# Optimization experiments

Hardware: AMD Instinct MI355X
Metric: run time of the kernel (lower is better)

## Reference

```python
import jax, jax.numpy as jnp
import numpy as np
import math

B, C, N, L = 32, 128, 2048, 1
H, DK, APT = 8, 16, 10
EPS = 1e-5


def conv1x1(x, W, b):
    # 1x1 Conv2d on [B, C, N, L]
    return jnp.einsum('oc,bcnl->bonl', W, x) + b[None, :, None, None]


def layer_norm_12(x):
    # normalize over dims (1, 2) as in the custom LayerNorm (no affine)
    mean = x.mean(axis=(1, 2), keepdims=True)
    var = x.var(axis=(1, 2), keepdims=True)
    return (x - mean) / jnp.sqrt(var + EPS)


def setup_inputs() -> dict:
    key = jax.random.key(0)
    ks = jax.random.split(key, 10)
    s = 0.05  # small-scale init for numerical stability
    inp = {
        'input': jax.random.normal(ks[0], (B, C, N, L), jnp.float32),
        'Wq': jax.random.normal(ks[1], (C, C), jnp.float32) * s,
        'bq': jnp.zeros((C,), jnp.float32),
        'Wv': jax.random.normal(ks[2], (C, C), jnp.float32) * s,
        'bv': jnp.zeros((C,), jnp.float32),
        'Wc': jax.random.normal(ks[3], (C, C), jnp.float32) * s,
        'bc': jnp.zeros((C,), jnp.float32),
        'memory': jax.random.normal(ks[4], (H, L, N, DK), jnp.float32) * s,
        'sa_weight': jnp.ones((C, N, L), jnp.float32),
        'sa_bias': jnp.zeros((C, N, L), jnp.float32),
        'nodevec1': jax.random.normal(ks[5], (N, APT), jnp.float32),
        'nodevec2': jax.random.normal(ks[6], (APT, N), jnp.float32),
        'Wg1': jax.random.normal(ks[7], (C, C), jnp.float32) * s,
        'bg1': jnp.zeros((C,), jnp.float32),
        'Wg2': jax.random.normal(ks[8], (C, C), jnp.float32) * s,
        'bg2': jnp.zeros((C,), jnp.float32),
        'Wg3': jax.random.normal(ks[9], (C, C), jnp.float32) * s,
        'bg3': jnp.zeros((C,), jnp.float32),
    }
    return inp


def reference(input, Wq, bq, Wv, bv, Wc, bc, memory, sa_weight, sa_bias,
              nodevec1, nodevec2, Wg1, bg1, Wg2, bg2, Wg3, bg3):
    scale = math.sqrt(DK)

    def split_heads(t):  # [B,C,N,L] -> [B,H,L,N,DK]
        return t.reshape(B, H, DK, N, L).transpose(0, 1, 4, 3, 2)

    # SpatialAttention (Conv = 1x1 conv + relu; dropout off in eval)
    q = jax.nn.relu(conv1x1(input, Wq, bq))
    v = jax.nn.relu(conv1x1(input, Wv, bv))
    query = jax.nn.softmax(split_heads(q) / scale, axis=-1)     # [B,H,L,N,DK]
    value = split_heads(v)                                       # [B,H,L,N,DK]
    key = jax.nn.softmax(memory / scale, axis=-1)                # [H,L,N,DK]
    Aapt = jax.nn.softmax(jax.nn.relu(nodevec1 @ nodevec2), axis=-1)  # [N,N]

    kv = jnp.einsum('hlnx,bhlny->bhlxy', key, value)             # [B,H,L,DK,DK]
    attn_qkv = jnp.einsum('bhlnx,bhlxy->bhlny', query, kv)       # [B,H,L,N,DK]
    attn_dyn = jnp.einsum('nm,bhlnc->bhlnc', Aapt, value)        # row-sum scaling
    x = attn_qkv + attn_dyn

    # merge heads back to [B,C,N,L] and apply concat conv (Conv = conv+relu)
    x = x.transpose(0, 1, 4, 3, 2).reshape(B, C, N, L)
    x = jax.nn.relu(conv1x1(x, Wc, bc))
    x = x * sa_weight[None] + sa_bias[None] + x                  # affine branch

    # Encoder wrap
    x = x + input
    x = layer_norm_12(x)
    g = conv1x1(x, Wg1, bg1) * jax.nn.sigmoid(conv1x1(x, Wg2, bg2))
    g = conv1x1(g, Wg3, bg3)                                     # GLU
    x = g + x
    x = x * sa_weight[None] + sa_bias[None] + x
    x = layer_norm_12(x)
    return x
```

## Files before the change

kernel.cpp:

```cpp
#include <hip/hip_runtime.h>
#include <hip/hip_bf16.h>
#include <math.h>

#define DI __device__ __forceinline__

typedef short bf16x8 __attribute__((ext_vector_type(8)));
typedef float f32x4 __attribute__((ext_vector_type(4)));

constexpr int BB = 32, CC = 128, NN = 2048;
constexpr float EPSf = 1e-5f;
constexpr float RCN = 1.0f / (CC * (float)NN);

#define MFMA(a,b,c) __builtin_amdgcn_mfma_f32_16x16x32_bf16(a,b,c,0,0,0)

DI unsigned short f2b(float f){
    union { __hip_bfloat16 h; unsigned short u; } v;
    v.h = __float2bfloat16(f);
    return v.u;
}
DI float b2f(unsigned short h){
    union { unsigned u; float f; } v; v.u = ((unsigned)h) << 16;
    return v.f;
}
DI float sigm(float x){ return 1.0f / (1.0f + __expf(-x)); }

__global__ __launch_bounds__(256) void k_prep(
    const float* __restrict__ Wq, const float* __restrict__ Wv,
    const float* __restrict__ Wc, const float* __restrict__ Wg1,
    const float* __restrict__ Wg2, const float* __restrict__ Wg3,
    const float* __restrict__ mem,
    unsigned short* __restrict__ Wb, float* __restrict__ rs,
    unsigned short* __restrict__ ksT)
{
    const int tid = threadIdx.x;
    if (blockIdx.x < 96) {
        const int i = blockIdx.x * 256 + tid;
        const int m = i >> 12, q = i & 4095;
        const float* src = (m==0)?Wq:(m==1)?Wv:(m==2)?Wc:(m==3)?Wg1:(m==4)?Wg2:Wg3;
        f32x4 w = *(const f32x4*)&src[q * 4];
        ushort4 p; p.x=f2b(w[0]); p.y=f2b(w[1]); p.z=f2b(w[2]); p.w=f2b(w[3]);
        *(ushort4*)&Wb[(size_t)m * 16384 + q * 4] = p;
    } else if (blockIdx.x == 96) {
        const float* src = (tid < 128) ? Wg1 : Wg2;
        const int o = tid & 127;
        float s = 0.f;
#pragma unroll
        for (int j = 0; j < 32; j++) {
            f32x4 a = *(const f32x4*)&src[o * 128 + j * 4];
            s += a[0] + a[1] + a[2] + a[3];
        }
        rs[tid] = s;
    } else {
        const int row = (blockIdx.x - 97) * 256 + tid;
        const int h = row >> 11, n = row & 2047;
        const float* p = mem + (size_t)row * 16;
        float v[16];
        f32x4 t0 = *(const f32x4*)(p);
        f32x4 t1 = *(const f32x4*)(p + 4);
        f32x4 t2 = *(const f32x4*)(p + 8);
        f32x4 t3 = *(const f32x4*)(p + 12);
#pragma unroll
        for (int j = 0; j < 4; j++) { v[j]=t0[j]; v[4+j]=t1[j]; v[8+j]=t2[j]; v[12+j]=t3[j]; }
        float mx = v[0];
#pragma unroll
        for (int x = 1; x < 16; x++) mx = fmaxf(mx, v[x]);
        float s = 0.f;
#pragma unroll
        for (int x = 0; x < 16; x++) { v[x] = __expf((v[x] - mx) * 0.25f); s += v[x]; }
        const float is = 1.0f / s;
#pragma unroll
        for (int x = 0; x < 16; x++)
            ksT[((size_t)(h * 16 + x)) * NN + n] = f2b(v[x] * is);
    }
}

__global__ __launch_bounds__(256,2) void k_qv(
    const float* __restrict__ in, const unsigned short* __restrict__ WqB,
    const unsigned short* __restrict__ WvB, const float* __restrict__ bq,
    const float* __restrict__ bv, unsigned short* __restrict__ qT,
    unsigned short* __restrict__ vT)
{
    __shared__ unsigned short tile[128 * 136];
    const int b = blockIdx.x >> 4, n0 = (blockIdx.x & 15) * 128;
    const int tid = threadIdx.x, l = tid & 63, wid = tid >> 6;
    const int wo = wid & 1, wn = wid >> 1, lr = l & 15, lg = l >> 4;
    f32x4 accq[4][4], accv[4][4];
    const f32x4 z = {0.f,0.f,0.f,0.f};
#pragma unroll
    for (int i = 0; i < 4; i++)
#pragma unroll
        for (int j = 0; j < 4; j++) { accq[i][j] = z; accv[i][j] = z; }
    const float* inb = in + (size_t)b * CC * NN;
#pragma unroll
    for (int ks = 0; ks < 4; ks++) {
        const int cb = ks * 32 + lg * 8;
        bf16x8 aq[4], av[4];
#pragma unroll
        for (int mf = 0; mf < 4; mf++) {
            const int o = wo*64 + mf*16 + lr;
            aq[mf] = *(const bf16x8*)&WqB[o * 128 + cb];
            av[mf] = *(const bf16x8*)&WvB[o * 128 + cb];
        }
        bf16x8 bx[4];
#pragma unroll
        for (int nf = 0; nf < 4; nf++) {
            const int n = n0 + wn*64 + nf*16 + lr;
            union { bf16x8 v; unsigned short u[8]; } t;
#pragma unroll
            for (int j = 0; j < 8; j++) t.u[j] = f2b(inb[(size_t)(cb + j) * NN + n]);
            bx[nf] = t.v;
        }
#pragma unroll
        for (int mf = 0; mf < 4; mf++)
#pragma unroll
            for (int nf = 0; nf < 4; nf++) {
                accq[mf][nf] = MFMA(aq[mf], bx[nf], accq[mf][nf]);
                accv[mf][nf] = MFMA(av[mf], bx[nf], accv[mf][nf]);
            }
    }
#pragma unroll
    for (int mf = 0; mf < 4; mf++) {
        const int ob = wo*64 + mf*16 + lg*4;
        const f32x4 b4 = *(const f32x4*)&bq[ob];
#pragma unroll
        for (int nf = 0; nf < 4; nf++) {
            const int nl = wn*64 + nf*16 + lr;
            f32x4 a = accq[mf][nf];
            ushort4 pk;
            pk.x = f2b(fmaxf(a[0]+b4[0],0.f)); pk.y = f2b(fmaxf(a[1]+b4[1],0.f));
            pk.z = f2b(fmaxf(a[2]+b4[2],0.f)); pk.w = f2b(fmaxf(a[3]+b4[3],0.f));
            *(ushort4*)&tile[nl * 136 + ob] = pk;
        }
    }
    __syncthreads();
#pragma unroll
    for (int p = 0; p < 8; p++) {
        const int row = p*16 + (tid >> 4), col = (tid & 15) * 8;
        *(uint4*)&qT[((size_t)b * NN + n0 + row) * CC + col] =
            *(const uint4*)&tile[row * 136 + col];
    }
    __syncthreads();
#pragma unroll
    for (int mf = 0; mf < 4; mf++) {
        const int ob = wo*64 + mf*16 + lg*4;
        const f32x4 b4 = *(const f32x4*)&bv[ob];
#pragma unroll
        for (int nf = 0; nf < 4; nf++) {
            const int nl = wn*64 + nf*16 + lr;
            f32x4 a = accv[mf][nf];
            ushort4 pk;
            pk.x = f2b(fmaxf(a[0]+b4[0],0.f)); pk.y = f2b(fmaxf(a[1]+b4[1],0.f));
            pk.z = f2b(fmaxf(a[2]+b4[2],0.f)); pk.w = f2b(fmaxf(a[3]+b4[3],0.f));
            *(ushort4*)&tile[nl * 136 + ob] = pk;
        }
    }
    __syncthreads();
#pragma unroll
    for (int p = 0; p < 8; p++) {
        const int row = p*16 + (tid >> 4), col = (tid & 15) * 8;
        *(uint4*)&vT[((size_t)b * NN + n0 + row) * CC + col] =
            *(const uint4*)&tile[row * 136 + col];
    }
}

__global__ __launch_bounds__(256) void k_kv(const unsigned short* __restrict__ ksT,
                                            const unsigned short* __restrict__ vT,
                                            float* __restrict__ kvb)
{
    __shared__ unsigned short vt[4 * 16 * 520];
    __shared__ float red[1024];
    const int b = blockIdx.x >> 3, h = blockIdx.x & 7;
    const int tid = threadIdx.x, l = tid & 63, wid = tid >> 6;
    const int n0 = wid * 512;
    unsigned short* vtw = vt + wid * (16 * 520);
    const unsigned short* vb = vT + ((size_t)b * NN + n0) * CC + h * 16;
#pragma unroll
    for (int r = 0; r < 8; r++) {
        const int nl = r * 64 + l;
        uint4 q0 = *(const uint4*)&vb[(size_t)nl * CC];
        uint4 q1 = *(const uint4*)&vb[(size_t)nl * CC + 8];
        const unsigned uu[8] = {q0.x,q0.y,q0.z,q0.w,q1.x,q1.y,q1.z,q1.w};
#pragma unroll
        for (int k = 0; k < 8; k++) {
            vtw[(2*k)*520 + nl]   = (unsigned short)(uu[k] & 0xffffu);
            vtw[(2*k+1)*520 + nl] = (unsigned short)(uu[k] >> 16);
        }
    }
    const int lr = l & 15, lg = l >> 4;
    const unsigned short* ka = ksT + (size_t)h * 16 * NN;
    f32x4 acc = {0.f,0.f,0.f,0.f};
#pragma unroll
    for (int kk = 0; kk < 16; kk++) {
        bf16x8 af = *(const bf16x8*)&ka[(size_t)lr * NN + n0 + kk*32 + lg*8];
        bf16x8 bf = *(const bf16x8*)&vtw[lr * 520 + kk*32 + lg*8];
        acc = MFMA(af, bf, acc);
    }
#pragma unroll
    for (int r = 0; r < 4; r++)
        red[wid * 256 + (lg*4 + r) * 16 + lr] = acc[r];
    __syncthreads();
    {
        const float s = red[tid] + red[256 + tid] + red[512 + tid] + red[768 + tid];
        kvb[((size_t)(b * 8 + h)) * 256 + tid] = s;
    }
}

__global__ __launch_bounds__(256,2) void k_attnC(
    const unsigned short* __restrict__ qT, unsigned short* __restrict__ vT,
    const float* __restrict__ kvb, const unsigned short* __restrict__ WcB,
    const float* __restrict__ bc, const float* __restrict__ saw,
    const float* __restrict__ sab, const float* __restrict__ in0f,
    float* __restrict__ part1)
{
    __shared__ float kvl[8 * 260];
    __shared__ unsigned short xc[128 * 136];
    __shared__ float red[8];
    const int b = blockIdx.x >> 4, n0 = (blockIdx.x & 15) * 128;
    const int tid = threadIdx.x;
    {
        const float* kp = kvb + (size_t)b * 2048 + (tid >> 5) * 256 + (tid & 31) * 8;
        f32x4 v0 = *(const f32x4*)kp;
        f32x4 v1 = *(const f32x4*)(kp + 4);
        float* dst = &kvl[(tid >> 5) * 260 + (tid & 31) * 8];
        *(f32x4*)dst = v0; *(f32x4*)(dst + 4) = v1;
    }
    __syncthreads();
#pragma unroll
    for (int it = 0; it < 4; it++) {
        const int idx = it * 256 + tid;
        const int nl = idx >> 3, h = idx & 7;
        const size_t base = ((size_t)b * NN + n0 + nl) * CC + h * 16;
        const unsigned short* qp = qT + base;
        const unsigned short* vp = vT + base;
        float q[16];
        {
            uint4 u0 = *(const uint4*)qp, u1 = *(const uint4*)(qp + 8);
            unsigned uu[8] = {u0.x,u0.y,u0.z,u0.w,u1.x,u1.y,u1.z,u1.w};
#pragma unroll
            for (int j = 0; j < 8; j++) {
                q[2*j]   = b2f((unsigned short)(uu[j] & 0xffffu));
                q[2*j+1] = b2f((unsigned short)(uu[j] >> 16));
            }
        }
        float mx = q[0];
#pragma unroll
        for (int x = 1; x < 16; x++) mx = fmaxf(mx, q[x]);
        float p[16]; float s = 0.f;
#pragma unroll
        for (int x = 0; x < 16; x++) { p[x] = __expf((q[x] - mx) * 0.25f); s += p[x]; }
        const float is = 1.0f / s;
        const float* kh = &kvl[h * 260];
        float r[16];
#pragma unroll
        for (int y = 0; y < 16; y++) r[y] = 0.f;
#pragma unroll
        for (int x = 0; x < 16; x++) {
            const float px = p[x];
#pragma unroll
            for (int y = 0; y < 16; y++) r[y] = fmaf(px, kh[x * 16 + y], r[y]);
        }
        uint4 w0 = *(const uint4*)vp, w1 = *(const uint4*)(vp + 8);
        unsigned vv[8] = {w0.x,w0.y,w0.z,w0.w,w1.x,w1.y,w1.z,w1.w};
        unsigned short* xp = &xc[nl * 136 + h * 16];
#pragma unroll
        for (int j2 = 0; j2 < 4; j2++) {
            ushort4 pk;
            pk.x = f2b(r[4*j2+0]*is + b2f((unsigned short)(vv[2*j2]   & 0xffffu)));
            pk.y = f2b(r[4*j2+1]*is + b2f((unsigned short)(vv[2*j2]   >> 16)));
            pk.z = f2b(r[4*j2+2]*is + b2f((unsigned short)(vv[2*j2+1] & 0xffffu)));
            pk.w = f2b(r[4*j2+3]*is + b2f((unsigned short)(vv[2*j2+1] >> 16)));
            *(ushort4*)&xp[j2 * 4] = pk;
        }
    }
    __syncthreads();
    const int l = tid & 63, wid = tid >> 6;
    const int wo = wid & 1, wn = wid >> 1, lr = l & 15, lg = l >> 4;
    f32x4 acc[4][4];
    const f32x4 z = {0.f,0.f,0.f,0.f};
#pragma unroll
    for (int i = 0; i < 4; i++)
#pragma unroll
        for (int j = 0; j < 4; j++) acc[i][j] = z;
#pragma unroll
    for (int ks = 0; ks < 4; ks++) {
        const int cb = ks * 32 + lg * 8;
        bf16x8 af[4];
#pragma unroll
        for (int mf = 0; mf < 4; mf++)
            af[mf] = *(const bf16x8*)&WcB[(wo*64 + mf*16 + lr) * 128 + cb];
        bf16x8 bx[4];
#pragma unroll
        for (int nf = 0; nf < 4; nf++)
            bx[nf] = *(const bf16x8*)&xc[(wn*64 + nf*16 + lr) * 136 + cb];
#pragma unroll
        for (int mf = 0; mf < 4; mf++)
#pragma unroll
            for (int nf = 0; nf < 4; nf++)
                acc[mf][nf] = MFMA(af[mf], bx[nf], acc[mf][nf]);
    }
    __syncthreads();
    float sum = 0.f, ssq = 0.f;
#pragma unroll
    for (int mf = 0; mf < 4; mf++) {
        const int ob = wo*64 + mf*16 + lg*4;
        const f32x4 b4 = *(const f32x4*)&bc[ob];
#pragma unroll
        for (int nf = 0; nf < 4; nf++) {
            const int nl = wn*64 + nf*16 + lr;
            const int n = n0 + nl;
            f32x4 a = acc[mf][nf];
            float ys[4];
#pragma unroll
            for (int r = 0; r < 4; r++) {
                const int o = ob + r;
                const float t = fmaxf(a[r] + b4[r], 0.f);
                const float sw = saw[(size_t)o * NN + n];
                const float sb = sab[(size_t)o * NN + n];
                float y = t * sw + sb + t + in0f[((size_t)b * CC + o) * NN + n];
                sum += y; ssq += y * y;
                ys[r] = y;
            }
            ushort4 pk;
            pk.x = f2b(ys[0]); pk.y = f2b(ys[1]); pk.z = f2b(ys[2]); pk.w = f2b(ys[3]);
            *(ushort4*)&xc[nl * 136 + ob] = pk;
        }
    }
    __syncthreads();
#pragma unroll
    for (int p = 0; p < 8; p++) {
        const int row = p*16 + (tid >> 4), col = (tid & 15) * 8;
        *(uint4*)&vT[((size_t)b * NN + n0 + row) * CC + col] =
            *(const uint4*)&xc[row * 136 + col];
    }
#pragma unroll
    for (int off = 32; off > 0; off >>= 1) {
        sum += __shfl_down(sum, off);
        ssq += __shfl_down(ssq, off);
    }
    if ((tid & 63) == 0) { red[wid*2] = sum; red[wid*2+1] = ssq; }
    __syncthreads();
    if (tid == 0) {
        part1[2 * blockIdx.x]     = red[0]+red[2]+red[4]+red[6];
        part1[2 * blockIdx.x + 1] = red[1]+red[3]+red[5]+red[7];
    }
}

__global__ __launch_bounds__(256,2) void k_glu3(
    const unsigned short* __restrict__ y1,
    const unsigned short* __restrict__ W1B, const unsigned short* __restrict__ W2B,
    const unsigned short* __restrict__ W3B,
    const float* __restrict__ b1, const float* __restrict__ b2,
    const float* __restrict__ b3, const float* __restrict__ rs,
    const float* __restrict__ part1, const float* __restrict__ saw,
    const float* __restrict__ sab, unsigned short* __restrict__ X2,
    float* __restrict__ part2)
{
    __shared__ unsigned short yt[128 * 136];
    __shared__ unsigned short gx[128 * 136];
    __shared__ float cs[256];
    __shared__ float red[8];
    const int b = blockIdx.x >> 4, n0 = (blockIdx.x & 15) * 128;
    const int tid = threadIdx.x;
    float s0 = 0.f, q0 = 0.f;
#pragma unroll
    for (int t = 0; t < 16; t++) { s0 += part1[(b*16+t)*2]; q0 += part1[(b*16+t)*2+1]; }
    const float mean = s0 * RCN;
    const float var  = q0 * RCN - mean * mean;
    const float inv  = rsqrtf(var + EPSf);
    {
        const int cq = tid & 15;
#pragma unroll
        for (int it = 0; it < 8; it++) {
            const int n = it * 16 + (tid >> 4);
            uint4 u = *(const uint4*)&y1[((size_t)b * NN + n0 + n) * CC + cq * 8];
            *(uint4*)&yt[n * 136 + cq * 8] = u;
        }
    }
    {
        const int o = tid & 127;
        const float bb = (tid < 128) ? b1[o] : b2[o];
        cs[tid] = bb - mean * inv * rs[tid];
    }
    __syncthreads();
    const int l = tid & 63, wid = tid >> 6;
    const int wo = wid & 1, wn = wid >> 1, lr = l & 15, lg = l >> 4;
    {
        f32x4 acc1[4][4], acc2[4][4];
        const f32x4 z = {0.f,0.f,0.f,0.f};
#pragma unroll
        for (int i = 0; i < 4; i++)
#pragma unroll
            for (int j = 0; j < 4; j++) { acc1[i][j] = z; acc2[i][j] = z; }
#pragma unroll
        for (int ks = 0; ks < 4; ks++) {
            const int cb = ks * 32 + lg * 8;
            bf16x8 a1[4], a2[4];
#pragma unroll
            for (int mf = 0; mf < 4; mf++) {
                const int o = wo*64 + mf*16 + lr;
                a1[mf] = *(const bf16x8*)&W1B[o * 128 + cb];
                a2[mf] = *(const bf16x8*)&W2B[o * 128 + cb];
            }
            bf16x8 bx[4];
#pragma unroll
            for (int nf = 0; nf < 4; nf++)
                bx[nf] = *(const bf16x8*)&yt[(wn*64 + nf*16 + lr) * 136 + cb];
#pragma unroll
            for (int mf = 0; mf < 4; mf++)
#pragma unroll
                for (int nf = 0; nf < 4; nf++) {
                    acc1[mf][nf] = MFMA(a1[mf], bx[nf], acc1[mf][nf]);
                    acc2[mf][nf] = MFMA(a2[mf], bx[nf], acc2[mf][nf]);
                }
        }
#pragma unroll
        for (int mf = 0; mf < 4; mf++) {
            const int ob = wo*64 + mf*16 + lg*4;
            const f32x4 c1 = *(const f32x4*)&cs[ob];
            const f32x4 c2 = *(const f32x4*)&cs[128 + ob];
#pragma unroll
            for (int nf = 0; nf < 4; nf++) {
                const int nl = wn*64 + nf*16 + lr;
                ushort4 pk;
                float g1, g2;
                g1 = acc1[mf][nf][0]*inv + c1[0]; g2 = acc2[mf][nf][0]*inv + c2[0];
                pk.x = f2b(g1 * sigm(g2));
                g1 = acc1[mf][nf][1]*inv + c1[1]; g2 = acc2[mf][nf][1]*inv + c2[1];
                pk.y = f2b(g1 * sigm(g2));
                g1 = acc1[mf][nf][2]*inv + c1[2]; g2 = acc2[mf][nf][2]*inv + c2[2];
                pk.z = f2b(g1 * sigm(g2));
                g1 = acc1[mf][nf][3]*inv + c1[3]; g2 = acc2[mf][nf][3]*inv + c2[3];
                pk.w = f2b(g1 * sigm(g2));
                *(ushort4*)&gx[nl * 136 + ob] = pk;
            }
        }
    }
    __syncthreads();
    f32x4 acc[4][4];
    const f32x4 z = {0.f,0.f,0.f,0.f};
#pragma unroll
    for (int i = 0; i < 4; i++)
#pragma unroll
        for (int j = 0; j < 4; j++) acc[i][j] = z;
#pragma unroll
    for (int ks = 0; ks < 4; ks++) {
        const int cb = ks * 32 + lg * 8;
        bf16x8 af[4];
#pragma unroll
        for (int mf = 0; mf < 4; mf++)
            af[mf] = *(const bf16x8*)&W3B[(wo*64 + mf*16 + lr) * 128 + cb];
        bf16x8 bx[4];
#pragma unroll
        for (int nf = 0; nf < 4; nf++)
            bx[nf] = *(const bf16x8*)&gx[(wn*64 + nf*16 + lr) * 136 + cb];
#pragma unroll
        for (int mf = 0; mf < 4; mf++)
#pragma unroll
            for (int nf = 0; nf < 4; nf++)
                acc[mf][nf] = MFMA(af[mf], bx[nf], acc[mf][nf]);
    }
    __syncthreads();
    float sum = 0.f, ssq = 0.f;
#pragma unroll
    for (int mf = 0; mf < 4; mf++) {
        const int ob = wo*64 + mf*16 + lg*4;
        const f32x4 b4 = *(const f32x4*)&b3[ob];
#pragma unroll
        for (int nf = 0; nf < 4; nf++) {
            const int nl = wn*64 + nf*16 + lr;
            const int n = n0 + nl;
            ushort4 yq = *(const ushort4*)&yt[nl * 136 + ob];
            f32x4 a = acc[mf][nf];
            float ys[4];
#pragma unroll
            for (int r = 0; r < 4; r++) {
                const int o = ob + r;
                const unsigned short ev = (r==0)?yq.x:(r==1)?yq.y:(r==2)?yq.z:yq.w;
                const float t = a[r] + b4[r] + (b2f(ev) - mean) * inv;
                const float sw = saw[(size_t)o * NN + n];
                const float sb = sab[(size_t)o * NN + n];
                const float y = t * sw + sb + t;
                sum += y; ssq += y * y;
                ys[r] = y;
            }
            ushort4 pk;
            pk.x = f2b(ys[0]); pk.y = f2b(ys[1]); pk.z = f2b(ys[2]); pk.w = f2b(ys[3]);
            *(ushort4*)&gx[nl * 136 + ob] = pk;
        }
    }
    __syncthreads();
#pragma unroll
    for (int p = 0; p < 8; p++) {
        const int row = p*16 + (tid >> 4), col = (tid & 15) * 8;
        *(uint4*)&X2[((size_t)b * NN + n0 + row) * CC + col] =
            *(const uint4*)&gx[row * 136 + col];
    }
#pragma unroll
    for (int off = 32; off > 0; off >>= 1) {
        sum += __shfl_down(sum, off);
        ssq += __shfl_down(ssq, off);
    }
    if ((tid & 63) == 0) { red[wid*2] = sum; red[wid*2+1] = ssq; }
    __syncthreads();
    if (tid == 0) {
        part2[2 * blockIdx.x]     = red[0]+red[2]+red[4]+red[6];
        part2[2 * blockIdx.x + 1] = red[1]+red[3]+red[5]+red[7];
    }
}

__global__ __launch_bounds__(256) void k_lnfin(const unsigned short* __restrict__ x2,
                                               const float* __restrict__ part2,
                                               float* __restrict__ out)
{
    __shared__ unsigned ts[64 * 69];
    const int b = blockIdx.x >> 5, n0 = (blockIdx.x & 31) * 64;
    const int tid = threadIdx.x;
    float s0 = 0.f, q0 = 0.f;
#pragma unroll
    for (int t = 0; t < 16; t++) { s0 += part2[(b*16+t)*2]; q0 += part2[(b*16+t)*2+1]; }
    const float mean = s0 * RCN;
    const float var  = q0 * RCN - mean * mean;
    const float inv  = rsqrtf(var + EPSf);
    {
        const int n = tid >> 2, qd = tid & 3;
        const unsigned short* src = x2 + ((size_t)b * NN + n0 + n) * CC + qd * 32;
        uint4 a0 = *(const uint4*)(src);
        uint4 a1 = *(const uint4*)(src + 8);
        uint4 a2 = *(const uint4*)(src + 16);
        uint4 a3 = *(const uint4*)(src + 24);
        unsigned u[16] = {a0.x,a0.y,a0.z,a0.w, a1.x,a1.y,a1.z,a1.w,
                          a2.x,a2.y,a2.z,a2.w, a3.x,a3.y,a3.z,a3.w};
#pragma unroll
        for (int k = 0; k < 16; k++)
            ts[(qd * 16 + k) * 69 + n] = u[k];
    }
    __syncthreads();
#pragma unroll
    for (int pass = 0; pass < 8; pass++) {
        const int c = pass * 16 + (tid >> 4), nq = tid & 15;
        const int cp = c >> 1, hi = c & 1;
        f32x4 v;
#pragma unroll
        for (int j = 0; j < 4; j++) {
            const unsigned u = ts[cp * 69 + nq * 4 + j];
            const unsigned short hv = hi ? (unsigned short)(u >> 16)
                                         : (unsigned short)(u & 0xffffu);
            v[j] = (b2f(hv) - mean) * inv;
        }
        *(f32x4*)&out[((size_t)b * CC + c) * NN + n0 + nq * 4] = v;
    }
}

extern "C" void kernel_launch(void* const* d_in, const int* in_sizes, int n_in,
                              void* d_out, int out_size, void* d_ws, size_t ws_size,
                              hipStream_t stream)
{
    const float* input = (const float*)d_in[0];
    const float* Wq  = (const float*)d_in[1];
    const float* bq  = (const float*)d_in[2];
    const float* Wv  = (const float*)d_in[3];
    const float* bv  = (const float*)d_in[4];
    const float* Wc  = (const float*)d_in[5];
    const float* bc  = (const float*)d_in[6];
    const float* mem = (const float*)d_in[7];
    const float* saw = (const float*)d_in[8];
    const float* sab = (const float*)d_in[9];
    const float* Wg1 = (const float*)d_in[12];
    const float* bg1 = (const float*)d_in[13];
    const float* Wg2 = (const float*)d_in[14];
    const float* bg2 = (const float*)d_in[15];
    const float* Wg3 = (const float*)d_in[16];
    const float* bg3 = (const float*)d_in[17];
    float* out = (float*)d_out;

    unsigned char* wsb = (unsigned char*)d_ws;
    unsigned short* qT  = (unsigned short*)(wsb);
    unsigned short* vT  = (unsigned short*)(wsb + 16777216);
    unsigned short* ksT = (unsigned short*)(wsb + 33554432);
    float* kvb   = (float*)(wsb + 34078720);
    unsigned short* Wb  = (unsigned short*)(wsb + 34340864);
    float* rs    = (float*)(wsb + 34537472);
    float* part1 = (float*)(wsb + 34538496);
    float* part2 = (float*)(wsb + 34542592);

    k_prep <<<161,  256, 0, stream>>>(Wq, Wv, Wc, Wg1, Wg2, Wg3, mem, Wb, rs, ksT);
    k_qv   <<<512,  256, 0, stream>>>(input, Wb, Wb + 16384, bq, bv, qT, vT);
    k_kv   <<<256,  256, 0, stream>>>(ksT, vT, kvb);
    k_attnC<<<512,  256, 0, stream>>>(qT, vT, kvb, Wb + 2*16384, bc, saw, sab,
                                      input, part1);
    k_glu3 <<<512,  256, 0, stream>>>(vT, Wb + 3*16384, Wb + 4*16384, Wb + 5*16384,
                                      bg1, bg2, bg3, rs, part1, saw, sab, qT, part2);
    k_lnfin<<<1024, 256, 0, stream>>>(qT, part2, out);
}
```

Before: 127.7 us.

## Stash bf16 transposed input in output buffer for residual; restructure softmax-kv loop

k_qv now writes the bf16-converted input tile, transposed to [B,N,C], into the output buffer as scratch. k_attnC reads the residual from that buffer as bf16 instead of re-reading the fp32 input with a strided column access. This halves the residual bytes and makes the reads coalesced, at the cost of an extra write pass and lower residual precision. The attention inner loop is also restructured to fuse exp and accumulation with vectorized LDS reads and no unroll, to cut register pressure.

```diff
diff --git a/kernel.cpp b/kernel.cpp
--- a/kernel.cpp
+++ b/kernel.cpp
@@ -78,7 +78,7 @@
     const float* __restrict__ in, const unsigned short* __restrict__ WqB,
     const unsigned short* __restrict__ WvB, const float* __restrict__ bq,
     const float* __restrict__ bv, unsigned short* __restrict__ qT,
-    unsigned short* __restrict__ vT)
+    unsigned short* __restrict__ vT, unsigned short* __restrict__ inT)
 {
     __shared__ unsigned short tile[128 * 136];
     const int b = blockIdx.x >> 4, n0 = (blockIdx.x & 15) * 128;
@@ -110,6 +110,11 @@
             for (int j = 0; j < 8; j++) t.u[j] = f2b(inb[(size_t)(cb + j) * NN + n]);
             bx[nf] = t.v;
         }
+        if (wo == 0) {
+#pragma unroll
+            for (int nf = 0; nf < 4; nf++)
+                *(bf16x8*)&tile[(wn*64 + nf*16 + lr) * 136 + cb] = bx[nf];
+        }
 #pragma unroll
         for (int mf = 0; mf < 4; mf++)
 #pragma unroll
@@ -118,6 +123,14 @@
                 accv[mf][nf] = MFMA(av[mf], bx[nf], accv[mf][nf]);
             }
     }
+    __syncthreads();
+#pragma unroll
+    for (int p = 0; p < 8; p++) {
+        const int row = p*16 + (tid >> 4), col = (tid & 15) * 8;
+        *(uint4*)&inT[((size_t)b * NN + n0 + row) * CC + col] =
+            *(const uint4*)&tile[row * 136 + col];
+    }
+    __syncthreads();
 #pragma unroll
     for (int mf = 0; mf < 4; mf++) {
         const int ob = wo*64 + mf*16 + lg*4;
@@ -209,7 +222,7 @@
     const unsigned short* __restrict__ qT, unsigned short* __restrict__ vT,
     const float* __restrict__ kvb, const unsigned short* __restrict__ WcB,
     const float* __restrict__ bc, const float* __restrict__ saw,
-    const float* __restrict__ sab, const float* __restrict__ in0f,
+    const float* __restrict__ sab, const unsigned short* __restrict__ inT,
     float* __restrict__ part1)
 {
     __shared__ float kvl[8 * 260];
@@ -225,50 +238,54 @@
         *(f32x4*)dst = v0; *(f32x4*)(dst + 4) = v1;
     }
     __syncthreads();
-#pragma unroll
+#pragma unroll 1
     for (int it = 0; it < 4; it++) {
         const int idx = it * 256 + tid;
         const int nl = idx >> 3, h = idx & 7;
         const size_t base = ((size_t)b * NN + n0 + nl) * CC + h * 16;
-        const unsigned short* qp = qT + base;
-        const unsigned short* vp = vT + base;
-        float q[16];
-        {
-            uint4 u0 = *(const uint4*)qp, u1 = *(const uint4*)(qp + 8);
-            unsigned uu[8] = {u0.x,u0.y,u0.z,u0.w,u1.x,u1.y,u1.z,u1.w};
-#pragma unroll
-            for (int j = 0; j < 8; j++) {
-                q[2*j]   = b2f((unsigned short)(uu[j] & 0xffffu));
-                q[2*j+1] = b2f((unsigned short)(uu[j] >> 16));
+        uint4 u0 = *(const uint4*)(qT + base);
+        uint4 u1 = *(const uint4*)(qT + base + 8);
+        uint4 w0 = *(const uint4*)(vT + base);
+        uint4 w1 = *(const uint4*)(vT + base + 8);
+        unsigned uu[8] = {u0.x,u0.y,u0.z,u0.w,u1.x,u1.y,u1.z,u1.w};
+        float mx = -1e30f;
+#pragma unroll
+        for (int j = 0; j < 8; j++) {
+            mx = fmaxf(mx, b2f((unsigned short)(uu[j] & 0xffffu)));
+            mx = fmaxf(mx, b2f((unsigned short)(uu[j] >> 16)));
+        }
+        const float* kh = &kvl[h * 260];
+        f32x4 r0 = {0,0,0,0}, r1 = {0,0,0,0}, r2 = {0,0,0,0}, r3 = {0,0,0,0};
+        float s = 0.f;
+#pragma unroll
+        for (int x = 0; x < 16; x++) {
+            const unsigned short qh = (x & 1) ? (unsigned short)(uu[x >> 1] >> 16)
+                                              : (unsigned short)(uu[x >> 1] & 0xffffu);
+            const float e = __expf((b2f(qh) - mx) * 0.25f);
+            s += e;
+            const f32x4 k0 = *(const f32x4*)&kh[x * 16];
+            const f32x4 k1 = *(const f32x4*)&kh[x * 16 + 4];
+            const f32x4 k2 = *(const f32x4*)&kh[x * 16 + 8];
+            const f32x4 k3 = *(const f32x4*)&kh[x * 16 + 12];
+#pragma unroll
+            for (int j = 0; j < 4; j++) {
+                r0[j] = fmaf(e, k0[j], r0[j]);
+                r1[j] = fmaf(e, k1[j], r1[j]);
+                r2[j] = fmaf(e, k2[j], r2[j]);
+                r3[j] = fmaf(e, k3[j], r3[j]);
             }
         }
-        float mx = q[0];
-#pragma unroll
-        for (int x = 1; x < 16; x++) mx = fmaxf(mx, q[x]);
-        float p[16]; float s = 0.f;
-#pragma unroll
-        for (int x = 0; x < 16; x++) { p[x] = __expf((q[x] - mx) * 0.25f); s += p[x]; }
         const float is = 1.0f / s;
-        const float* kh = &kvl[h * 260];
-        float r[16];
-#pragma unroll
-        for (int y = 0; y < 16; y++) r[y] = 0.f;
-#pragma unroll
-        for (int x = 0; x < 16; x++) {
-            const float px = p[x];
-#pragma unroll
-            for (int y = 0; y < 16; y++) r[y] = fmaf(px, kh[x * 16 + y], r[y]);
-        }
-        uint4 w0 = *(const uint4*)vp, w1 = *(const uint4*)(vp + 8);
         unsigned vv[8] = {w0.x,w0.y,w0.z,w0.w,w1.x,w1.y,w1.z,w1.w};
         unsigned short* xp = &xc[nl * 136 + h * 16];
 #pragma unroll
         for (int j2 = 0; j2 < 4; j2++) {
+            const f32x4 rr = (j2==0)?r0:(j2==1)?r1:(j2==2)?r2:r3;
             ushort4 pk;
-            pk.x = f2b(r[4*j2+0]*is + b2f((unsigned short)(vv[2*j2]   & 0xffffu)));
-            pk.y = f2b(r[4*j2+1]*is + b2f((unsigned short)(vv[2*j2]   >> 16)));
-            pk.z = f2b(r[4*j2+2]*is + b2f((unsigned short)(vv[2*j2+1] & 0xffffu)));
-            pk.w = f2b(r[4*j2+3]*is + b2f((unsigned short)(vv[2*j2+1] >> 16)));
+            pk.x = f2b(rr[0]*is + b2f((unsigned short)(vv[2*j2]   & 0xffffu)));
+            pk.y = f2b(rr[1]*is + b2f((unsigned short)(vv[2*j2]   >> 16)));
+            pk.z = f2b(rr[2]*is + b2f((unsigned short)(vv[2*j2+1] & 0xffffu)));
+            pk.w = f2b(rr[3]*is + b2f((unsigned short)(vv[2*j2+1] >> 16)));
             *(ushort4*)&xp[j2 * 4] = pk;
         }
     }
@@ -309,6 +326,7 @@
             const int nl = wn*64 + nf*16 + lr;
             const int n = n0 + nl;
             f32x4 a = acc[mf][nf];
+            const ushort4 iu = *(const ushort4*)&inT[((size_t)b * NN + n) * CC + ob];
             float ys[4];
 #pragma unroll
             for (int r = 0; r < 4; r++) {
@@ -316,7 +334,8 @@
                 const float t = fmaxf(a[r] + b4[r], 0.f);
                 const float sw = saw[(size_t)o * NN + n];
                 const float sb = sab[(size_t)o * NN + n];
-                float y = t * sw + sb + t + in0f[((size_t)b * CC + o) * NN + n];
+                const unsigned short iv = (r==0)?iu.x:(r==1)?iu.y:(r==2)?iu.z:iu.w;
+                float y = t * sw + sb + t + b2f(iv);
                 sum += y; ssq += y * y;
                 ys[r] = y;
             }
@@ -582,12 +601,13 @@
     float* rs    = (float*)(wsb + 34537472);
     float* part1 = (float*)(wsb + 34538496);
     float* part2 = (float*)(wsb + 34542592);
+    unsigned short* inT = (unsigned short*)d_out;
 
     k_prep <<<161,  256, 0, stream>>>(Wq, Wv, Wc, Wg1, Wg2, Wg3, mem, Wb, rs, ksT);
-    k_qv   <<<512,  256, 0, stream>>>(input, Wb, Wb + 16384, bq, bv, qT, vT);
+    k_qv   <<<512,  256, 0, stream>>>(input, Wb, Wb + 16384, bq, bv, qT, vT, inT);
     k_kv   <<<256,  256, 0, stream>>>(ksT, vT, kvb);
     k_attnC<<<512,  256, 0, stream>>>(qT, vT, kvb, Wb + 2*16384, bc, saw, sab,
-                                      input, part1);
+                                      inT, part1);
     k_glu3 <<<512,  256, 0, stream>>>(vT, Wb + 3*16384, Wb + 4*16384, Wb + 5*16384,
                                       bg1, bg2, bg3, rs, part1, saw, sab, qT, part2);
     k_lnfin<<<1024, 256, 0, stream>>>(qT, part2, out);
```

Measured after the change: 115.2 us. -9.8%, faster.
